# Kernel tuning notes

Hardware: AMD Instinct MI355X
Metric: run time of the kernel (lower is better)

## Reference

```python
import jax, jax.numpy as jnp
import numpy as np

E, TOPK, H, F, CAP, TP = 8, 2, 1024, 4096, 2048, 1
N = 8192  # tokens * topk (token copies)


def setup_inputs() -> dict:
    key = jax.random.key(0)
    ks = jax.random.split(key, 6)
    inputs_shard = jax.random.normal(ks[0], (N, H), jnp.float32)
    gate_weight = jax.random.uniform(ks[1], (N,), jnp.float32)
    choosed_experts = jax.random.randint(ks[2], (N,), 0, E, dtype=jnp.int32)
    new_index = jax.random.permutation(ks[3], N).astype(jnp.int32)
    w1 = jax.random.normal(ks[4], (E, F, H), jnp.float32) * 0.02
    w2 = jax.random.normal(ks[5], (E, H, F), jnp.float32) * 0.02
    return {"inputs_shard": inputs_shard, "gate_weight": gate_weight,
            "choosed_experts": choosed_experts, "new_index": new_index,
            "w1": w1, "w2": w2}


def _grouped_expert_mlp(x, experts, w1, w2):
    # capacity-based grouped GEMM: sort token copies by expert, pack into
    # (E, CAP, H), run batched fc1->gelu->fc2, unpack back to token order.
    n = x.shape[0]
    order = jnp.argsort(experts)                      # [N]
    se = experts[order]
    offsets = jnp.searchsorted(se, jnp.arange(E))     # start of each expert block
    rank = jnp.arange(n) - offsets[se]                # within-expert position
    valid = rank < CAP                                # CAP=2*N/E, ~never drops
    slot = jnp.where(valid, se * CAP + rank, E * CAP) # out-of-range -> dropped
    buf = jnp.zeros((E * CAP, x.shape[1]), x.dtype).at[slot].set(x[order], mode="drop")
    xe = buf.reshape(E, CAP, -1)                      # [E, CAP, H]
    h = jax.nn.gelu(jnp.einsum("ech,efh->ecf", xe, w1), approximate=False)
    ye = jnp.einsum("ecf,ehf->ech", h, w2).reshape(E * CAP, -1)
    y_sorted = jnp.where(valid[:, None], ye[jnp.clip(slot, 0, E * CAP - 1)], 0.0)
    return jnp.zeros_like(x).at[order].set(y_sorted)  # back to token-copy order


def reference(inputs_shard, gate_weight, choosed_experts, new_index, w1, w2):
    # expert compute, scaled by router probabilities (combine-side scaling)
    result = _grouped_expert_mlp(inputs_shard, choosed_experts, w1, w2)
    result = result * gate_weight[:, None]
    # scatter combine: output1[new_index] = result; full_output += output1
    full_output = jnp.zeros((N, H), result.dtype).at[new_index].set(result)
    # topk reduce: view(N//topk, topk, H).sum(1)
    topk_reduce = full_output.reshape(N // TOPK, TOPK, H).sum(1)
    # reduce_scatter over TP group; TP=1 => identity
    return topk_reduce
```

## Files before the change

### kernel.cpp

```cpp
#include <hip/hip_runtime.h>
#include <stdint.h>

#define N_TOK 8192
#define HDIM  1024
#define FDIM  4096
#define NEXP  8
#define MAXTILES 72
#define MAXT256  40

typedef __attribute__((ext_vector_type(8))) __bf16 bf16x8;
typedef __attribute__((ext_vector_type(8))) unsigned short ushort8v;
typedef __attribute__((ext_vector_type(4))) unsigned short ushort4v;
typedef __attribute__((ext_vector_type(4))) float floatx4;

__device__ __forceinline__ unsigned short f2bf(float f) {
  union { float f; uint32_t u; } v; v.f = f;
  uint32_t u = v.u;
  return (unsigned short)((u + 0x7FFFu + ((u >> 16) & 1u)) >> 16);
}

__device__ __forceinline__ void load_lds16(const void* g, void* l) {
  __builtin_amdgcn_global_load_lds(
      (const __attribute__((address_space(1))) void*)(uintptr_t)g,
      (__attribute__((address_space(3))) void*)(uint32_t)(uintptr_t)l,
      16, 0, 0);
}


__global__ void k_count(const int* __restrict__ experts, int* __restrict__ meta) {
  int i = blockIdx.x * 256 + threadIdx.x;
  atomicAdd(&meta[experts[i]], 1);
}

__global__ void k_plan(int* __restrict__ meta) {
  if (threadIdx.x == 0) {
    int off = 0, nt = 0, nt2 = 0;
    for (int e = 0; e < NEXP; ++e) {
      int c = meta[e];
      meta[8 + e] = off;
      meta[16 + e] = off;
      int t = (c + 127) >> 7;
      for (int k = 0; k < t; ++k) meta[32 + nt++] = (e << 16) | k;
      int t2 = (c + 255) >> 8;
      for (int k = 0; k < t2; ++k) meta[104 + nt2++] = (e << 16) | k;
      off += c;
    }
    meta[24] = nt;
    meta[25] = nt2;
  }
}

__global__ void k_scatter(const int* __restrict__ experts, int* __restrict__ meta,
                          int* __restrict__ order) {
  int i = blockIdx.x * 256 + threadIdx.x;
  int e = experts[i];
  int pos = atomicAdd(&meta[16 + e], 1);
  order[pos] = i;
}

__global__ void k_pack(const float* __restrict__ x, const int* __restrict__ order,
                       unsigned short* __restrict__ xs) {
  int s = blockIdx.x;
  int i = order[s];
  int t = threadIdx.x;
  float4 v = *(const float4*)(x + (size_t)i * HDIM + t * 4);
  ushort4v u;
  u[0] = f2bf(v.x); u[1] = f2bf(v.y); u[2] = f2bf(v.z); u[3] = f2bf(v.w);
  *(ushort4v*)(xs + (size_t)s * HDIM + t * 4) = u;
}

__global__ void k_cvt(const float* __restrict__ src, unsigned short* __restrict__ dst) {
  size_t i = ((size_t)blockIdx.x * 256 + threadIdx.x) * 4;
  float4 v = *(const float4*)(src + i);
  ushort4v u;
  u[0] = f2bf(v.x); u[1] = f2bf(v.y); u[2] = f2bf(v.z); u[3] = f2bf(v.w);
  *(ushort4v*)(dst + i) = u;
}


#define VM_WAIT(n) asm volatile("s_waitcnt vmcnt(" #n ")" ::: "memory")

template <int K_TOTAL, int NT, int EPI>
__global__ __launch_bounds__(512, 1) void gemm_big(
    const unsigned short* __restrict__ A, const unsigned short* __restrict__ B,
    unsigned short* __restrict__ h1out, const float* __restrict__ gate,
    const int* __restrict__ new_index, float* __restrict__ out,
    const int* __restrict__ meta) {
  __shared__ unsigned short As[3][256 * 64];
  __shared__ unsigned short Bs[3][128 * 64];

  int bx = blockIdx.z;
  if (bx >= meta[25]) return;
  int entry = meta[104 + bx];
  int e = entry >> 16, mt = entry & 0xffff;
  int row0 = meta[8 + e] + mt * 256;
  int rend = meta[8 + e] + meta[e];
  int nBase = blockIdx.x * 128;
  int kStart = blockIdx.y * (NT * 64);

  int tid = threadIdx.x;
  int w = tid >> 6, l = tid & 63;
  int r = l & 15, q = l >> 4;

  int srow = w * 8 + (l >> 3);
  int scol = ((l & 7) ^ (l >> 3)) << 3;
  const unsigned short* aP[4];
  const unsigned short* bP[2];
#pragma unroll
  for (int n = 0; n < 4; ++n) {
    int ar = min(row0 + n * 64 + srow, N_TOK - 1);
    aP[n] = A + (size_t)ar * K_TOTAL + kStart + scol;
  }
#pragma unroll
  for (int n = 0; n < 2; ++n) {
    int br = nBase + n * 64 + srow;
    bP[n] = B + (size_t)e * 4194304 + (size_t)br * K_TOTAL + kStart + scol;
  }

  floatx4 acc[4][4];
#pragma unroll
  for (int i = 0; i < 4; ++i)
#pragma unroll
    for (int j = 0; j < 4; ++j) acc[i][j] = (floatx4){0.f, 0.f, 0.f, 0.f};

  int mb = (w >> 1) * 64;
  int nb = (w & 1) * 64;

#pragma unroll
  for (int n = 0; n < 4; ++n) load_lds16(aP[n], &As[0][n * 4096 + w * 512]);
#pragma unroll
  for (int n = 0; n < 2; ++n) load_lds16(bP[n], &Bs[0][n * 4096 + w * 512]);
#pragma unroll
  for (int n = 0; n < 4; ++n) load_lds16(aP[n] + 64, &As[1][n * 4096 + w * 512]);
#pragma unroll
  for (int n = 0; n < 2; ++n) load_lds16(bP[n] + 64, &Bs[1][n * 4096 + w * 512]);

  int cur = 0;
  for (int kt = 0; kt < NT; ++kt) {
    if (kt == NT - 1) { VM_WAIT(0); } else { VM_WAIT(6); }
    __builtin_amdgcn_s_barrier();
    __builtin_amdgcn_sched_barrier(0);

    if (kt + 2 < NT) {
      int stg = cur + 2; if (stg >= 3) stg -= 3;
      int ko = (kt + 2) * 64;
#pragma unroll
      for (int n = 0; n < 4; ++n) load_lds16(aP[n] + ko, &As[stg][n * 4096 + w * 512]);
#pragma unroll
      for (int n = 0; n < 2; ++n) load_lds16(bP[n] + ko, &Bs[stg][n * 4096 + w * 512]);
    }

#pragma unroll
    for (int kk = 0; kk < 2; ++kk) {
      bf16x8 av[4], bv[4];
#pragma unroll
      for (int i = 0; i < 4; ++i) {
        int row = mb + i * 16 + r;
        int col = (kk * 32 + q * 8) ^ ((r & 7) << 3);
        av[i] = __builtin_bit_cast(bf16x8, *(const ushort8v*)&As[cur][row * 64 + col]);
      }
#pragma unroll
      for (int j = 0; j < 4; ++j) {
        int row = nb + j * 16 + r;
        int col = (kk * 32 + q * 8) ^ ((r & 7) << 3);
        bv[j] = __builtin_bit_cast(bf16x8, *(const ushort8v*)&Bs[cur][row * 64 + col]);
      }
      __builtin_amdgcn_s_setprio(1);
#pragma unroll
      for (int i = 0; i < 4; ++i)
#pragma unroll
        for (int j = 0; j < 4; ++j)
          acc[i][j] = __builtin_amdgcn_mfma_f32_16x16x32_bf16(av[i], bv[j], acc[i][j], 0, 0, 0);
      __builtin_amdgcn_s_setprio(0);
    }

    ++cur; if (cur >= 3) cur = 0;
  }

  if constexpr (EPI == 0) {
#pragma unroll
    for (int i = 0; i < 4; ++i) {
      int mrow = row0 + mb + i * 16 + q * 4;
#pragma unroll
      for (int reg = 0; reg < 4; ++reg) {
        int s = mrow + reg;
        if (s < rend) {
          unsigned short* dst = h1out + (size_t)s * FDIM + nBase + nb + r;
#pragma unroll
          for (int j = 0; j < 4; ++j) {
            float v = acc[i][j][reg];
            float g = 0.5f * v * (1.0f + erff(v * 0.70710678118654752f));
            dst[j * 16] = f2bf(g);
          }
        }
      }
    }
  } else {
    const int* order = meta + 256;
#pragma unroll
    for (int i = 0; i < 4; ++i) {
      int mrow = row0 + mb + i * 16 + q * 4;
#pragma unroll
      for (int reg = 0; reg < 4; ++reg) {
        int s = mrow + reg;
        if (s < rend) {
          int itok = order[s];
          float gw = gate[itok];
          int jdx = new_index[itok];
          float* dst = out + (size_t)(jdx >> 1) * HDIM + nBase + nb + r;
#pragma unroll
          for (int j = 0; j < 4; ++j) atomicAdd(dst + j * 16, acc[i][j][reg] * gw);
        }
      }
    }
  }
}


template <bool PRE>
__global__ __launch_bounds__(256) void gemm1_t(
    const unsigned short* __restrict__ xs, const void* __restrict__ w1v,
    unsigned short* __restrict__ h1, const int* __restrict__ meta) {
  __shared__ unsigned short As[128 * 32];
  __shared__ unsigned short Bs[128 * 32];

  int bx = blockIdx.z;
  if (bx >= meta[24]) return;
  int entry = meta[32 + bx];
  int e = entry >> 16, mt = entry & 0xffff;
  int row0 = meta[8 + e] + mt * 128;
  int rend = meta[8 + e] + meta[e];
  int fBase = blockIdx.x * 128;

  int tid = threadIdx.x;
  int w = tid >> 6, lane = tid & 63;
  int r = lane & 15, q = lane >> 4;
  int wm = (w >> 1) * 64, wn = (w & 1) * 64;

  int ar0 = (w * 16) + (lane >> 2);
  int s0 = min(row0 + ar0, N_TOK - 1);
  int s1 = min(row0 + 64 + ar0, N_TOK - 1);
  const unsigned short* ag0 = xs + (size_t)s0 * HDIM + (lane & 3) * 8;
  const unsigned short* ag1 = xs + (size_t)s1 * HDIM + (lane & 3) * 8;
  unsigned short* al0 = &As[(w * 16) * 32];
  unsigned short* al1 = &As[(64 + w * 16) * 32];

  const float* wbase = nullptr; int brow = 0, bkk = 0;
  brow = tid >> 1; bkk = (tid & 1) * 16;
  wbase = (const float*)w1v + ((size_t)e * FDIM + fBase + brow) * HDIM + bkk;

  floatx4 acc[4][4];
#pragma unroll
  for (int i = 0; i < 4; ++i)
#pragma unroll
    for (int j = 0; j < 4; ++j) acc[i][j] = (floatx4){0.f, 0.f, 0.f, 0.f};

  for (int k0 = 0; k0 < HDIM; k0 += 32) {
    __syncthreads();
    load_lds16(ag0 + k0, al0);
    load_lds16(ag1 + k0, al1);
    {
      const float* gb = wbase + k0;
      float4 f0 = *(const float4*)(gb);
      float4 f1 = *(const float4*)(gb + 4);
      float4 f2 = *(const float4*)(gb + 8);
      float4 f3 = *(const float4*)(gb + 12);
      ushort8v u0, u1;
      u0[0] = f2bf(f0.x); u0[1] = f2bf(f0.y); u0[2] = f2bf(f0.z); u0[3] = f2bf(f0.w);
      u0[4] = f2bf(f1.x); u0[5] = f2bf(f1.y); u0[6] = f2bf(f1.z); u0[7] = f2bf(f1.w);
      u1[0] = f2bf(f2.x); u1[1] = f2bf(f2.y); u1[2] = f2bf(f2.z); u1[3] = f2bf(f2.w);
      u1[4] = f2bf(f3.x); u1[5] = f2bf(f3.y); u1[6] = f2bf(f3.z); u1[7] = f2bf(f3.w);
      *(ushort8v*)&Bs[brow * 32 + bkk] = u0;
      *(ushort8v*)&Bs[brow * 32 + bkk + 8] = u1;
    }
    __syncthreads();

    bf16x8 av[4], bv[4];
#pragma unroll
    for (int i = 0; i < 4; ++i)
      av[i] = __builtin_bit_cast(bf16x8, *(const ushort8v*)&As[(wm + i * 16 + r) * 32 + q * 8]);
#pragma unroll
    for (int j = 0; j < 4; ++j)
      bv[j] = __builtin_bit_cast(bf16x8, *(const ushort8v*)&Bs[(wn + j * 16 + r) * 32 + q * 8]);
#pragma unroll
    for (int i = 0; i < 4; ++i)
#pragma unroll
      for (int j = 0; j < 4; ++j)
        acc[i][j] = __builtin_amdgcn_mfma_f32_16x16x32_bf16(av[i], bv[j], acc[i][j], 0, 0, 0);
  }

#pragma unroll
  for (int i = 0; i < 4; ++i) {
    int mrow = row0 + wm + i * 16 + q * 4;
#pragma unroll
    for (int reg = 0; reg < 4; ++reg) {
      int s = mrow + reg;
      if (s < rend) {
        unsigned short* dst = h1 + (size_t)s * FDIM + fBase + wn + r;
#pragma unroll
        for (int j = 0; j < 4; ++j) {
          float v = acc[i][j][reg];
          float g = 0.5f * v * (1.0f + erff(v * 0.70710678118654752f));
          dst[j * 16] = f2bf(g);
        }
      }
    }
  }
}

template <bool PRE>
__global__ __launch_bounds__(256) void gemm2_t(
    const unsigned short* __restrict__ h1, const void* __restrict__ w2v,
    const float* __restrict__ gate, const int* __restrict__ new_index,
    float* __restrict__ out, const int* __restrict__ meta) {
  __shared__ unsigned short As[128 * 32];
  __shared__ unsigned short Bs[128 * 32];

  int bx = blockIdx.z;
  if (bx >= meta[24]) return;
  int entry = meta[32 + bx];
  int e = entry >> 16, mt = entry & 0xffff;
  int row0 = meta[8 + e] + mt * 128;
  int rend = meta[8 + e] + meta[e];
  int nBase = blockIdx.x * 128;
  int kStart = blockIdx.y * (FDIM / 2);
  int kEnd = kStart + (FDIM / 2);
  const int* order = meta + 256;

  int tid = threadIdx.x;
  int w = tid >> 6, lane = tid & 63;
  int r = lane & 15, q = lane >> 4;
  int wm = (w >> 1) * 64, wn = (w & 1) * 64;

  int ar0 = (w * 16) + (lane >> 2);
  int s0 = min(row0 + ar0, N_TOK - 1);
  int s1 = min(row0 + 64 + ar0, N_TOK - 1);
  const unsigned short* ag0 = h1 + (size_t)s0 * FDIM + (lane & 3) * 8;
  const unsigned short* ag1 = h1 + (size_t)s1 * FDIM + (lane & 3) * 8;
  unsigned short* al0 = &As[(w * 16) * 32];
  unsigned short* al1 = &As[(64 + w * 16) * 32];

  const float* wbase = nullptr; int brow = 0, bkk = 0;
  brow = tid >> 1; bkk = (tid & 1) * 16;
  wbase = (const float*)w2v + ((size_t)e * HDIM + nBase + brow) * FDIM + bkk;

  floatx4 acc[4][4];
#pragma unroll
  for (int i = 0; i < 4; ++i)
#pragma unroll
    for (int j = 0; j < 4; ++j) acc[i][j] = (floatx4){0.f, 0.f, 0.f, 0.f};

  for (int k0 = kStart; k0 < kEnd; k0 += 32) {
    __syncthreads();
    load_lds16(ag0 + k0, al0);
    load_lds16(ag1 + k0, al1);
    {
      const float* gb = wbase + k0;
      float4 f0 = *(const float4*)(gb);
      float4 f1 = *(const float4*)(gb + 4);
      float4 f2 = *(const float4*)(gb + 8);
      float4 f3 = *(const float4*)(gb + 12);
      ushort8v u0, u1;
      u0[0] = f2bf(f0.x); u0[1] = f2bf(f0.y); u0[2] = f2bf(f0.z); u0[3] = f2bf(f0.w);
      u0[4] = f2bf(f1.x); u0[5] = f2bf(f1.y); u0[6] = f2bf(f1.z); u0[7] = f2bf(f1.w);
      u1[0] = f2bf(f2.x); u1[1] = f2bf(f2.y); u1[2] = f2bf(f2.z); u1[3] = f2bf(f2.w);
      u1[4] = f2bf(f3.x); u1[5] = f2bf(f3.y); u1[6] = f2bf(f3.z); u1[7] = f2bf(f3.w);
      *(ushort8v*)&Bs[brow * 32 + bkk] = u0;
      *(ushort8v*)&Bs[brow * 32 + bkk + 8] = u1;
    }
    __syncthreads();

    bf16x8 av[4], bv[4];
#pragma unroll
    for (int i = 0; i < 4; ++i)
      av[i] = __builtin_bit_cast(bf16x8, *(const ushort8v*)&As[(wm + i * 16 + r) * 32 + q * 8]);
#pragma unroll
    for (int j = 0; j < 4; ++j)
      bv[j] = __builtin_bit_cast(bf16x8, *(const ushort8v*)&Bs[(wn + j * 16 + r) * 32 + q * 8]);
#pragma unroll
    for (int i = 0; i < 4; ++i)
#pragma unroll
      for (int j = 0; j < 4; ++j)
        acc[i][j] = __builtin_amdgcn_mfma_f32_16x16x32_bf16(av[i], bv[j], acc[i][j], 0, 0, 0);
  }

#pragma unroll
  for (int i = 0; i < 4; ++i) {
    int mrow = row0 + wm + i * 16 + q * 4;
#pragma unroll
    for (int reg = 0; reg < 4; ++reg) {
      int s = mrow + reg;
      if (s < rend) {
        int itok = order[s];
        float gw = gate[itok];
        int jdx = new_index[itok];
        float* dst = out + (size_t)(jdx >> 1) * HDIM + nBase + wn + r;
#pragma unroll
        for (int j = 0; j < 4; ++j) atomicAdd(dst + j * 16, acc[i][j][reg] * gw);
      }
    }
  }
}

extern "C" void kernel_launch(void* const* d_in, const int* in_sizes, int n_in,
                              void* d_out, int out_size, void* d_ws, size_t ws_size,
                              hipStream_t stream) {
  const float* x        = (const float*)d_in[0];
  const float* gate     = (const float*)d_in[1];
  const int* experts    = (const int*)d_in[2];
  const int* new_index  = (const int*)d_in[3];
  const float* w1       = (const float*)d_in[4];
  const float* w2       = (const float*)d_in[5];
  float* out            = (float*)d_out;

  int* meta = (int*)d_ws;
  int* order = meta + 256;
  const size_t XS_OFF = 65536;
  const size_t XS_SZ  = (size_t)N_TOK * HDIM * 2;
  const size_t H1_SZ  = (size_t)N_TOK * FDIM * 2;
  const size_t W_SZ   = (size_t)NEXP * FDIM * HDIM * 2;
  unsigned short* xs  = (unsigned short*)((char*)d_ws + XS_OFF);
  unsigned short* h1  = (unsigned short*)((char*)d_ws + XS_OFF + XS_SZ);
  unsigned short* w1b = (unsigned short*)((char*)d_ws + XS_OFF + XS_SZ + H1_SZ);
  unsigned short* w2b = (unsigned short*)((char*)d_ws + XS_OFF + XS_SZ + H1_SZ + W_SZ);
  size_t need_small = XS_OFF + XS_SZ + H1_SZ;
  size_t need_big   = need_small + 2 * W_SZ;
  if (ws_size < need_small) return;
  bool big = ws_size >= need_big;

  hipMemsetAsync(d_ws, 0, 4096, stream);
  hipMemsetAsync(d_out, 0, (size_t)out_size * sizeof(float), stream);
  k_count<<<N_TOK / 256, 256, 0, stream>>>(experts, meta);
  k_plan<<<1, 64, 0, stream>>>(meta);
  k_scatter<<<N_TOK / 256, 256, 0, stream>>>(experts, meta, order);
  k_pack<<<N_TOK, 256, 0, stream>>>(x, order, xs);

  if (big) {
    int nblk = (int)((size_t)NEXP * FDIM * HDIM / 4 / 256);
    k_cvt<<<nblk, 256, 0, stream>>>(w1, w1b);
    k_cvt<<<nblk, 256, 0, stream>>>(w2, w2b);
    gemm_big<HDIM, 16, 0><<<dim3(FDIM / 128, 1, MAXT256), 512, 0, stream>>>(
        xs, w1b, h1, nullptr, nullptr, nullptr, meta);
    gemm_big<FDIM, 32, 1><<<dim3(HDIM / 128, 2, MAXT256), 512, 0, stream>>>(
        h1, w2b, nullptr, gate, new_index, out, meta);
  } else {
    gemm1_t<false><<<dim3(FDIM / 128, 1, MAXTILES), 256, 0, stream>>>(xs, w1, h1, meta);
    gemm2_t<false><<<dim3(HDIM / 128, 2, MAXTILES), 256, 0, stream>>>(h1, w2, gate, new_index, out, meta);
  }
}
```

Baseline: 676.5 us.

## Halve GEMM K-tile to raise occupancy and fuse routing prep kernels

Three routing kernels (count, plan, scatter) and a workspace memset are replaced by one 1024-thread kernel that counts experts in LDS, builds the tile plan, and scatters the order array. The big GEMM's K-tile shrinks from 64 to 32, with a matching 4-way swizzle and doubled iteration counts. LDS per block drops to about half, and launch bounds are raised to allow several blocks per CU. The goal is more waves per CU for latency hiding, at the cost of more barriers per unit of K and possible register pressure.

```diff
diff --git a/kernel.cpp b/kernel.cpp
--- a/kernel.cpp
+++ b/kernel.cpp
@@ -27,18 +27,29 @@
 }
 
 
-__global__ void k_count(const int* __restrict__ experts, int* __restrict__ meta) {
-  int i = blockIdx.x * 256 + threadIdx.x;
-  atomicAdd(&meta[experts[i]], 1);
-}
-
-__global__ void k_plan(int* __restrict__ meta) {
-  if (threadIdx.x == 0) {
+__global__ __launch_bounds__(1024) void k_prep(const int* __restrict__ experts,
+                                               int* __restrict__ meta,
+                                               int* __restrict__ order) {
+  __shared__ int cnt[NEXP];
+  __shared__ int base[NEXP];
+  int tid = threadIdx.x;
+  if (tid < NEXP) cnt[tid] = 0;
+  __syncthreads();
+  int eloc[8];
+#pragma unroll
+  for (int k = 0; k < 8; ++k) {
+    int e = experts[tid + k * 1024];
+    eloc[k] = e;
+    atomicAdd(&cnt[e], 1);
+  }
+  __syncthreads();
+  if (tid == 0) {
     int off = 0, nt = 0, nt2 = 0;
     for (int e = 0; e < NEXP; ++e) {
-      int c = meta[e];
+      int c = cnt[e];
+      meta[e] = c;
       meta[8 + e] = off;
-      meta[16 + e] = off;
+      base[e] = off;
       int t = (c + 127) >> 7;
       for (int k = 0; k < t; ++k) meta[32 + nt++] = (e << 16) | k;
       int t2 = (c + 255) >> 8;
@@ -48,14 +59,14 @@
     meta[24] = nt;
     meta[25] = nt2;
   }
-}
-
-__global__ void k_scatter(const int* __restrict__ experts, int* __restrict__ meta,
-                          int* __restrict__ order) {
-  int i = blockIdx.x * 256 + threadIdx.x;
-  int e = experts[i];
-  int pos = atomicAdd(&meta[16 + e], 1);
-  order[pos] = i;
+  __syncthreads();
+  if (tid < NEXP) cnt[tid] = base[tid];
+  __syncthreads();
+#pragma unroll
+  for (int k = 0; k < 8; ++k) {
+    int pos = atomicAdd(&cnt[eloc[k]], 1);
+    order[pos] = tid + k * 1024;
+  }
 }
 
 __global__ void k_pack(const float* __restrict__ x, const int* __restrict__ order,
@@ -81,13 +92,13 @@
 #define VM_WAIT(n) asm volatile("s_waitcnt vmcnt(" #n ")" ::: "memory")
 
 template <int K_TOTAL, int NT, int EPI>
-__global__ __launch_bounds__(512, 1) void gemm_big(
+__global__ __launch_bounds__(512, 4) void gemm_big(
     const unsigned short* __restrict__ A, const unsigned short* __restrict__ B,
     unsigned short* __restrict__ h1out, const float* __restrict__ gate,
     const int* __restrict__ new_index, float* __restrict__ out,
     const int* __restrict__ meta) {
-  __shared__ unsigned short As[3][256 * 64];
-  __shared__ unsigned short Bs[3][128 * 64];
+  __shared__ unsigned short As[3][256 * 32];
+  __shared__ unsigned short Bs[3][128 * 32];
 
   int bx = blockIdx.z;
   if (bx >= meta[25]) return;
@@ -96,25 +107,24 @@
   int row0 = meta[8 + e] + mt * 256;
   int rend = meta[8 + e] + meta[e];
   int nBase = blockIdx.x * 128;
-  int kStart = blockIdx.y * (NT * 64);
+  int kStart = blockIdx.y * (NT * 32);
 
   int tid = threadIdx.x;
   int w = tid >> 6, l = tid & 63;
   int r = l & 15, q = l >> 4;
 
-  int srow = w * 8 + (l >> 3);
-  int scol = ((l & 7) ^ (l >> 3)) << 3;
-  const unsigned short* aP[4];
-  const unsigned short* bP[2];
-#pragma unroll
-  for (int n = 0; n < 4; ++n) {
-    int ar = min(row0 + n * 64 + srow, N_TOK - 1);
+  int srow = w * 16 + (l >> 2);
+  int scol = ((l & 3) ^ ((l >> 2) & 3)) << 3;
+  const unsigned short* aP[2];
+  const unsigned short* bP;
+#pragma unroll
+  for (int n = 0; n < 2; ++n) {
+    int ar = min(row0 + n * 128 + srow, N_TOK - 1);
     aP[n] = A + (size_t)ar * K_TOTAL + kStart + scol;
   }
-#pragma unroll
-  for (int n = 0; n < 2; ++n) {
-    int br = nBase + n * 64 + srow;
-    bP[n] = B + (size_t)e * 4194304 + (size_t)br * K_TOTAL + kStart + scol;
+  {
+    int br = nBase + srow;
+    bP = B + (size_t)e * 4194304 + (size_t)br * K_TOTAL + kStart + scol;
   }
 
   floatx4 acc[4][4];
@@ -127,43 +137,38 @@
   int nb = (w & 1) * 64;
 
 #pragma unroll
-  for (int n = 0; n < 4; ++n) load_lds16(aP[n], &As[0][n * 4096 + w * 512]);
-#pragma unroll
-  for (int n = 0; n < 2; ++n) load_lds16(bP[n], &Bs[0][n * 4096 + w * 512]);
-#pragma unroll
-  for (int n = 0; n < 4; ++n) load_lds16(aP[n] + 64, &As[1][n * 4096 + w * 512]);
-#pragma unroll
-  for (int n = 0; n < 2; ++n) load_lds16(bP[n] + 64, &Bs[1][n * 4096 + w * 512]);
+  for (int n = 0; n < 2; ++n) load_lds16(aP[n], &As[0][(n * 128 + w * 16) * 32]);
+  load_lds16(bP, &Bs[0][(w * 16) * 32]);
+#pragma unroll
+  for (int n = 0; n < 2; ++n) load_lds16(aP[n] + 32, &As[1][(n * 128 + w * 16) * 32]);
+  load_lds16(bP + 32, &Bs[1][(w * 16) * 32]);
 
   int cur = 0;
   for (int kt = 0; kt < NT; ++kt) {
-    if (kt == NT - 1) { VM_WAIT(0); } else { VM_WAIT(6); }
+    if (kt == NT - 1) { VM_WAIT(0); } else { VM_WAIT(3); }
     __builtin_amdgcn_s_barrier();
     __builtin_amdgcn_sched_barrier(0);
 
     if (kt + 2 < NT) {
       int stg = cur + 2; if (stg >= 3) stg -= 3;
-      int ko = (kt + 2) * 64;
-#pragma unroll
-      for (int n = 0; n < 4; ++n) load_lds16(aP[n] + ko, &As[stg][n * 4096 + w * 512]);
-#pragma unroll
-      for (int n = 0; n < 2; ++n) load_lds16(bP[n] + ko, &Bs[stg][n * 4096 + w * 512]);
-    }
-
-#pragma unroll
-    for (int kk = 0; kk < 2; ++kk) {
+      int ko = (kt + 2) * 32;
+#pragma unroll
+      for (int n = 0; n < 2; ++n) load_lds16(aP[n] + ko, &As[stg][(n * 128 + w * 16) * 32]);
+      load_lds16(bP + ko, &Bs[stg][(w * 16) * 32]);
+    }
+
+    {
       bf16x8 av[4], bv[4];
+      int col = (q ^ (r & 3)) * 8;
 #pragma unroll
       for (int i = 0; i < 4; ++i) {
         int row = mb + i * 16 + r;
-        int col = (kk * 32 + q * 8) ^ ((r & 7) << 3);
-        av[i] = __builtin_bit_cast(bf16x8, *(const ushort8v*)&As[cur][row * 64 + col]);
+        av[i] = __builtin_bit_cast(bf16x8, *(const ushort8v*)&As[cur][row * 32 + col]);
       }
 #pragma unroll
       for (int j = 0; j < 4; ++j) {
         int row = nb + j * 16 + r;
-        int col = (kk * 32 + q * 8) ^ ((r & 7) << 3);
-        bv[j] = __builtin_bit_cast(bf16x8, *(const ushort8v*)&Bs[cur][row * 64 + col]);
+        bv[j] = __builtin_bit_cast(bf16x8, *(const ushort8v*)&Bs[cur][row * 32 + col]);
       }
       __builtin_amdgcn_s_setprio(1);
 #pragma unroll
@@ -428,20 +433,17 @@
   if (ws_size < need_small) return;
   bool big = ws_size >= need_big;
 
-  hipMemsetAsync(d_ws, 0, 4096, stream);
   hipMemsetAsync(d_out, 0, (size_t)out_size * sizeof(float), stream);
-  k_count<<<N_TOK / 256, 256, 0, stream>>>(experts, meta);
-  k_plan<<<1, 64, 0, stream>>>(meta);
-  k_scatter<<<N_TOK / 256, 256, 0, stream>>>(experts, meta, order);
+  k_prep<<<1, 1024, 0, stream>>>(experts, meta, order);
   k_pack<<<N_TOK, 256, 0, stream>>>(x, order, xs);
 
   if (big) {
     int nblk = (int)((size_t)NEXP * FDIM * HDIM / 4 / 256);
     k_cvt<<<nblk, 256, 0, stream>>>(w1, w1b);
     k_cvt<<<nblk, 256, 0, stream>>>(w2, w2b);
-    gemm_big<HDIM, 16, 0><<<dim3(FDIM / 128, 1, MAXT256), 512, 0, stream>>>(
+    gemm_big<HDIM, 32, 0><<<dim3(FDIM / 128, 1, MAXT256), 512, 0, stream>>>(
         xs, w1b, h1, nullptr, nullptr, nullptr, meta);
-    gemm_big<FDIM, 32, 1><<<dim3(HDIM / 128, 2, MAXT256), 512, 0, stream>>>(
+    gemm_big<FDIM, 64, 1><<<dim3(HDIM / 128, 2, MAXT256), 512, 0, stream>>>(
         h1, w2b, nullptr, gate, new_index, out, meta);
   } else {
     gemm1_t<false><<<dim3(FDIM / 128, 1, MAXTILES), 256, 0, stream>>>(xs, w1, h1, meta);
```

Measured after the change: 583.4 us. -13.8%, faster.
